# Kernel tuning notes

Hardware: AMD Instinct MI355X
Metric: run time of the kernel (lower is better)

Reference implementation:

```python
import jax, jax.numpy as jnp
import numpy as np

NOISE_STD = 0.5   # quantization_noise_std default in PSN.run
BETA = 0.25       # commitment-loss weight
B, E, C, K = 64, 256, 256, 8192


def setup_inputs() -> dict:
    key = jax.random.key(0)
    k1, k2, k3 = jax.random.split(key, 3)
    latents = jax.random.normal(k1, (B, E, C), dtype=jnp.float32)
    # initial_codebook: uniform(-1, 1) then mean-centered over the code axis
    codebook = jax.random.uniform(k2, (K, C), dtype=jnp.float32, minval=-1.0, maxval=1.0)
    codebook = codebook - codebook.mean(axis=0)
    noise = jax.random.normal(k3, (B * E, 1), dtype=jnp.float32)
    return {"latents": latents, "codebook": codebook, "noise": noise}


def reference(latents, codebook, noise):
    b, e, c = latents.shape
    k = codebook.shape[0]
    flat = latents.reshape(b * e, c)                      # (b s) (r c), r=1
    dist = (jnp.sum(flat * flat, axis=1, keepdims=True)
            + jnp.sum(codebook * codebook, axis=1)
            - 2.0 * jnp.matmul(flat, codebook.T))
    inds_det = jnp.argmin(dist, axis=1)                   # [N]
    offs = jnp.round(noise[:, 0] * NOISE_STD).astype(jnp.int32)
    inds_noisy = jnp.clip(inds_det.astype(jnp.int32) + offs, 0, k - 1)
    # one-hot @ codebook == gather (same math, same vjp scatter-add)
    q_det = codebook[inds_det].reshape(b, e, c)
    q_noisy = codebook[inds_noisy].reshape(b, e, c)
    # straight-through estimator output fed to the post-quantizer
    st = latents + jax.lax.stop_gradient(q_noisy - latents)
    # non_recon_loss(latents, q_det, q_noisy): beta*mse(latents, sg(q_det)) + mse(q_noisy, sg(latents))
    loss = (BETA * jnp.mean((latents - jax.lax.stop_gradient(q_det)) ** 2)
            + jnp.mean((q_noisy - jax.lax.stop_gradient(latents)) ** 2))
    return st, loss, inds_noisy.reshape(b, e)
```

## Files before the change

kernel.cpp:

```cpp
#include <hip/hip_runtime.h>
#include <hip/hip_bf16.h>


namespace {
constexpr int N_ROWS  = 16384;
constexpr int K_CODES = 8192;
constexpr int C_DIM   = 256;
constexpr float EPS_GAP = 0.004f;
}

typedef __attribute__((ext_vector_type(8)))  short bf16x8;
typedef __attribute__((ext_vector_type(16))) float f32x16;

typedef __attribute__((address_space(1))) const unsigned int gas_u32;
typedef __attribute__((address_space(3))) unsigned int las_u32;

__device__ __forceinline__ void gld16(const unsigned short* g, unsigned short* l) {
    __builtin_amdgcn_global_load_lds((gas_u32*)g, (las_u32*)l, 16, 0, 0);
}

__device__ __forceinline__ unsigned f2key(float f) {
    unsigned u = __float_as_uint(f);
    return (u & 0x80000000u) ? ~u : (u | 0x80000000u);
}
__device__ __forceinline__ float key2f(unsigned k) {
    unsigned u = (k & 0x80000000u) ? (k ^ 0x80000000u) : ~k;
    return __uint_as_float(u);
}
__device__ __forceinline__ unsigned short f2bf(float x) {
    unsigned u = __float_as_uint(x);
    unsigned r = u + 0x7fffu + ((u >> 16) & 1u);
    return (unsigned short)(r >> 16);
}

extern "C" __global__ void prep_kernel(const float* __restrict__ src,
                                       unsigned short* __restrict__ hi,
                                       unsigned short* __restrict__ lo) {
    const int i = (blockIdx.x * 256 + threadIdx.x) * 8;
    const int row = i >> 8, col = i & 255;
    const int d = (((row >> 5) * 8 + (col >> 5)) * 4 + ((col >> 3) & 3)) * 256
                + (row & 31) * 8;
    float4 a = *(const float4*)&src[i];
    float4 b = *(const float4*)&src[i + 4];
    float v[8] = {a.x, a.y, a.z, a.w, b.x, b.y, b.z, b.w};
    unsigned short h[8], l[8];
    #pragma unroll
    for (int j = 0; j < 8; ++j) {
        h[j] = f2bf(v[j]);
        float hf = __uint_as_float((unsigned)h[j] << 16);
        l[j] = f2bf(v[j] - hf);
    }
    ushort4 h0 = {h[0], h[1], h[2], h[3]}, h1 = {h[4], h[5], h[6], h[7]};
    ushort4 l0 = {l[0], l[1], l[2], l[3]}, l1 = {l[4], l[5], l[6], l[7]};
    *(ushort4*)&hi[d] = h0;  *(ushort4*)&hi[d + 4] = h1;
    *(ushort4*)&lo[d] = l0;  *(ushort4*)&lo[d + 4] = l1;
}

extern "C" __global__ void prepw_kernel(const float* __restrict__ src,
                                        unsigned short* __restrict__ hi,
                                        unsigned short* __restrict__ lo,
                                        float* __restrict__ wnorm) {
    const int i = (blockIdx.x * 256 + threadIdx.x) * 8;
    float4 a = *(const float4*)&src[i];
    float4 b = *(const float4*)&src[i + 4];
    float v[8] = {a.x, a.y, a.z, a.w, b.x, b.y, b.z, b.w};
    unsigned short h[8], l[8];
    float s = 0.0f;
    #pragma unroll
    for (int j = 0; j < 8; ++j) {
        h[j] = f2bf(v[j]);
        float hf = __uint_as_float((unsigned)h[j] << 16);
        l[j] = f2bf(v[j] - hf);
        s = fmaf(v[j], v[j], s);
    }
    ushort4 h0 = {h[0], h[1], h[2], h[3]}, h1 = {h[4], h[5], h[6], h[7]};
    ushort4 l0 = {l[0], l[1], l[2], l[3]}, l1 = {l[4], l[5], l[6], l[7]};
    *(ushort4*)&hi[i] = h0;  *(ushort4*)&hi[i + 4] = h1;
    *(ushort4*)&lo[i] = l0;  *(ushort4*)&lo[i + 4] = l1;
    #pragma unroll
    for (int m = 1; m < 32; m <<= 1) s += __shfl_xor(s, m, 64);
    if ((threadIdx.x & 31) == 0) wnorm[i >> 8] = s;
}

extern "C" __global__ void __launch_bounds__(256, 3)
pass1_kernel(const unsigned short* __restrict__ xh_g,
             const unsigned short* __restrict__ xl_g,
             const unsigned short* __restrict__ wh_g,
             const unsigned short* __restrict__ wl_g,
             const float* __restrict__ wnorm,
             unsigned long long* __restrict__ keys,
             unsigned* __restrict__ keys2) {
    __shared__ __align__(16) unsigned short LDS[2][2][128 * 32];
    const int tid = threadIdx.x;
    const int lane = tid & 63;
    const int wid = tid >> 6;
    const int h = lane >> 5;
    const int l31 = lane & 31;
    const int rb = blockIdx.x & 127, cs = blockIdx.x >> 7;
    const int r0 = rb * 128, cbase = cs * 512;

    const int dr = lane >> 2;
    const int gq = (lane & 3) ^ ((lane >> 3) & 3);
    const int laneoff = dr * 256 + gq * 8;

    const int fB = (l31 >> 1) & 3;

    const size_t abase = ((size_t)(rb * 4 + wid) * 8) * 1024 + h * 256 + l31 * 8;

    float bv[16];  unsigned bi[16];  float sv[16];
    #pragma unroll
    for (int r = 0; r < 16; ++r) { bv[r] = 3.4e38f; sv[r] = 3.4e38f; bi[r] = 0; }

    f32x16 acc[4];
    #pragma unroll
    for (int g = 0; g < 4; ++g)
        #pragma unroll
        for (int e = 0; e < 16; ++e) acc[g][e] = 0.0f;

    auto stageW = [&](int t, int b) {
        const int kc32 = (t & 7) * 32;
        const int cb = cbase + (t >> 3) * 128;
        #pragma unroll
        for (int c = 0; c < 2; ++c) {
            const int R = wid * 32 + c * 16;
            const size_t wg = (size_t)(cb + R) * 256 + kc32 + laneoff;
            gld16(wh_g + wg, &LDS[b][0][R * 32]);
            gld16(wl_g + wg, &LDS[b][1][R * 32]);
        }
    };

    bf16x8 cAh0, cAh1, cAl0, cAl1;
    bf16x8 nAh0, nAh1, nAl0, nAl1;

#define LOADA(H0, H1, L0, L1, tt)                                              \
    {   const size_t o_ = abase + (size_t)((tt) & 7) * 1024;                   \
        H0 = *(const bf16x8*)(xh_g + o_);                                      \
        H1 = *(const bf16x8*)(xh_g + o_ + 512);                                \
        L0 = *(const bf16x8*)(xl_g + o_);                                      \
        L1 = *(const bf16x8*)(xl_g + o_ + 512);                                \
    }

#define MFMA_TILE(H0, H1, L0, L1, P)                                           \
    {   _Pragma("unroll")                                                      \
        for (int kk = 0; kk < 2; ++kk) {                                       \
            const int q = kk * 2 + h;                                          \
            bf16x8 ah = kk ? H1 : H0;                                          \
            bf16x8 al = kk ? L1 : L0;                                          \
            _Pragma("unroll")                                                  \
            for (int g = 0; g < 4; ++g) {                                      \
                const int aB = (g * 32 + l31) * 32 + ((q ^ fB) << 3);          \
                bf16x8 bh = *(const bf16x8*)&LDS[P][0][aB];                    \
                bf16x8 bl = *(const bf16x8*)&LDS[P][1][aB];                    \
                acc[g] = __builtin_amdgcn_mfma_f32_32x32x16_bf16(ah, bh, acc[g], 0, 0, 0); \
                acc[g] = __builtin_amdgcn_mfma_f32_32x32x16_bf16(ah, bl, acc[g], 0, 0, 0); \
                acc[g] = __builtin_amdgcn_mfma_f32_32x32x16_bf16(al, bh, acc[g], 0, 0, 0); \
            }                                                                  \
        }                                                                      \
    }

    auto epilogue = [&](int t) {
        const int cb = cbase + (t >> 3) * 128;
        float wn0 = wnorm[cb + l31];
        float wn1 = wnorm[cb + 32 + l31];
        float wn2 = wnorm[cb + 64 + l31];
        float wn3 = wnorm[cb + 96 + l31];
        #pragma unroll
        for (int r = 0; r < 16; ++r) {
            #pragma unroll
            for (int g = 0; g < 4; ++g) {
                const float wn = g == 0 ? wn0 : g == 1 ? wn1 : g == 2 ? wn2 : wn3;
                float s = fmaf(-2.0f, acc[g][r], wn);
                bool c = s < bv[r];
                sv[r] = fminf(sv[r], c ? bv[r] : s);
                bv[r] = c ? s : bv[r];
                bi[r] = c ? (unsigned)(cb + g * 32 + l31) : bi[r];
            }
        }
        #pragma unroll
        for (int g = 0; g < 4; ++g)
            #pragma unroll
            for (int e = 0; e < 16; ++e) acc[g][e] = 0.0f;
    };

    stageW(0, 0);
    LOADA(cAh0, cAh1, cAl0, cAl1, 0);
    __syncthreads();
    for (int t2 = 0; t2 < 32; t2 += 2) {
        stageW(t2 + 1, 1);
        LOADA(nAh0, nAh1, nAl0, nAl1, t2 + 1);
        MFMA_TILE(cAh0, cAh1, cAl0, cAl1, 0);
        __syncthreads();

        if (t2 + 2 < 32) {
            stageW(t2 + 2, 0);
            LOADA(cAh0, cAh1, cAl0, cAl1, t2 + 2);
        }
        MFMA_TILE(nAh0, nAh1, nAl0, nAl1, 1);
        if (((t2 + 1) & 7) == 7) epilogue(t2 + 1);
        __syncthreads();
    }
#undef LOADA
#undef MFMA_TILE

    #pragma unroll
    for (int r = 0; r < 16; ++r) {
        unsigned long long key =
            ((unsigned long long)f2key(bv[r]) << 32) | bi[r];
        unsigned sk = f2key(sv[r]);
        #pragma unroll
        for (int m = 1; m < 32; m <<= 1) {
            unsigned long long ko = __shfl_xor(key, m, 64);
            unsigned sko = __shfl_xor(sk, m, 64);
            unsigned long long loser = key < ko ? ko : key;
            sk = min(min(sk, sko), (unsigned)(loser >> 32));
            key = key < ko ? key : ko;
        }
        if (l31 == 0) {
            const int grow = r0 + wid * 32 + (r & 3) + 8 * (r >> 2) + 4 * h;
            unsigned long long old = atomicMin(&keys[grow], key);
            if (old != ~0ull) {
                unsigned long long loser = old < key ? key : old;
                atomicMin(&keys2[grow], (unsigned)(loser >> 32));
            }
            atomicMin(&keys2[grow], sk);
        }
    }
}

extern "C" __global__ void flag_kernel(unsigned long long* __restrict__ keys,
                                       const unsigned* __restrict__ keys2,
                                       int* __restrict__ list, int* __restrict__ count) {
    const int row = blockIdx.x * 256 + threadIdx.x;
    unsigned long long k = keys[row];
    float b = key2f((unsigned)(k >> 32));
    float s = key2f(keys2[row]);
    if (s - b < EPS_GAP) {
        int p = atomicAdd(count, 1);
        list[p] = row;
        keys[row] = ~0ull;
    }
}

extern "C" __global__ void __launch_bounds__(256)
rerank_kernel(const float* __restrict__ lat,
              const float* __restrict__ cbk,
              const float* __restrict__ wnorm,
              const int* __restrict__ list,
              const int* __restrict__ count,
              unsigned long long* __restrict__ keys) {
    const int w = threadIdx.x >> 6, lane = threadIdx.x & 63;
    const int c0 = blockIdx.x * 16 + w * 4;
    float4 wv0 = *(const float4*)&cbk[(size_t)(c0 + 0) * C_DIM + lane * 4];
    float4 wv1 = *(const float4*)&cbk[(size_t)(c0 + 1) * C_DIM + lane * 4];
    float4 wv2 = *(const float4*)&cbk[(size_t)(c0 + 2) * C_DIM + lane * 4];
    float4 wv3 = *(const float4*)&cbk[(size_t)(c0 + 3) * C_DIM + lane * 4];
    const float wn0 = wnorm[c0 + 0], wn1 = wnorm[c0 + 1];
    const float wn2 = wnorm[c0 + 2], wn3 = wnorm[c0 + 3];
    const int n = *count;

    auto dot4 = [&](const float4& x, const float4& v) {
        float d = x.x * v.x;
        d = fmaf(x.y, v.y, d);
        d = fmaf(x.z, v.z, d);
        return fmaf(x.w, v.w, d);
    };
    auto best4 = [&](float a0, float a1, float a2, float a3) {
        unsigned long long k0 = ((unsigned long long)f2key(fmaf(-2.0f, a0, wn0)) << 32) | (unsigned)(c0 + 0);
        unsigned long long k1 = ((unsigned long long)f2key(fmaf(-2.0f, a1, wn1)) << 32) | (unsigned)(c0 + 1);
        unsigned long long k2 = ((unsigned long long)f2key(fmaf(-2.0f, a2, wn2)) << 32) | (unsigned)(c0 + 2);
        unsigned long long k3 = ((unsigned long long)f2key(fmaf(-2.0f, a3, wn3)) << 32) | (unsigned)(c0 + 3);
        unsigned long long b01 = k0 < k1 ? k0 : k1;
        unsigned long long b23 = k2 < k3 ? k2 : k3;
        return b01 < b23 ? b01 : b23;
    };

    int i = 0;
    for (; i + 2 <= n; i += 2) {
        const int r0 = list[i], r1 = list[i + 1];
        float4 x0 = *(const float4*)&lat[(size_t)r0 * C_DIM + lane * 4];
        float4 x1 = *(const float4*)&lat[(size_t)r1 * C_DIM + lane * 4];
        float d00 = dot4(x0, wv0), d01 = dot4(x0, wv1), d02 = dot4(x0, wv2), d03 = dot4(x0, wv3);
        float d10 = dot4(x1, wv0), d11 = dot4(x1, wv1), d12 = dot4(x1, wv2), d13 = dot4(x1, wv3);
        #pragma unroll
        for (int m = 1; m < 64; m <<= 1) {
            d00 += __shfl_xor(d00, m, 64); d01 += __shfl_xor(d01, m, 64);
            d02 += __shfl_xor(d02, m, 64); d03 += __shfl_xor(d03, m, 64);
            d10 += __shfl_xor(d10, m, 64); d11 += __shfl_xor(d11, m, 64);
            d12 += __shfl_xor(d12, m, 64); d13 += __shfl_xor(d13, m, 64);
        }
        if (lane == 0) {
            unsigned long long b0 = best4(d00, d01, d02, d03);
            unsigned long long b1 = best4(d10, d11, d12, d13);
            if (b0 < keys[r0]) atomicMin(&keys[r0], b0);
            if (b1 < keys[r1]) atomicMin(&keys[r1], b1);
        }
    }
    if (i < n) {
        const int r0 = list[i];
        float4 x0 = *(const float4*)&lat[(size_t)r0 * C_DIM + lane * 4];
        float d00 = dot4(x0, wv0), d01 = dot4(x0, wv1), d02 = dot4(x0, wv2), d03 = dot4(x0, wv3);
        #pragma unroll
        for (int m = 1; m < 64; m <<= 1) {
            d00 += __shfl_xor(d00, m, 64); d01 += __shfl_xor(d01, m, 64);
            d02 += __shfl_xor(d02, m, 64); d03 += __shfl_xor(d03, m, 64);
        }
        if (lane == 0) {
            unsigned long long b0 = best4(d00, d01, d02, d03);
            if (b0 < keys[r0]) atomicMin(&keys[r0], b0);
        }
    }
}

extern "C" __global__ void finalize_kernel(const float* __restrict__ lat,
                                           const float* __restrict__ cbk,
                                           const float* __restrict__ noise,
                                           const unsigned long long* __restrict__ keys,
                                           float* __restrict__ out,
                                           float* __restrict__ lpart) {
    const int g = threadIdx.x >> 5;
    const int l = threadIdx.x & 31;
    const int row = blockIdx.x * 8 + g;
    const unsigned long long p = keys[row];
    const int id = (int)(unsigned)(p & 0xFFFFFFFFull);
    const int off = (int)rintf(noise[row] * 0.5f);
    int idn = id + off;
    idn = idn < 0 ? 0 : (idn > K_CODES - 1 ? K_CODES - 1 : idn);
    const float4* latp = (const float4*)&lat[(size_t)row * C_DIM];
    const float4* qdp  = (const float4*)&cbk[(size_t)id  * C_DIM];
    const float4* qnp  = (const float4*)&cbk[(size_t)idn * C_DIM];
    float4* stp = (float4*)&out[(size_t)row * C_DIM];
    float t = 0.0f;
    #pragma unroll
    for (int j = 0; j < 2; ++j) {
        const int e = l + j * 32;
        float4 x  = latp[e];
        float4 qd = qdp[e];
        float4 qn = qnp[e];
        float4 st = {x.x + (qn.x - x.x), x.y + (qn.y - x.y),
                     x.z + (qn.z - x.z), x.w + (qn.w - x.w)};
        stp[e] = st;
        float d1, d2;
        d1 = x.x - qd.x; d2 = qn.x - x.x; t += 0.25f * d1 * d1 + d2 * d2;
        d1 = x.y - qd.y; d2 = qn.y - x.y; t += 0.25f * d1 * d1 + d2 * d2;
        d1 = x.z - qd.z; d2 = qn.z - x.z; t += 0.25f * d1 * d1 + d2 * d2;
        d1 = x.w - qd.w; d2 = qn.w - x.w; t += 0.25f * d1 * d1 + d2 * d2;
    }
    t *= (1.0f / 4194304.0f);
    #pragma unroll
    for (int m = 1; m < 32; m <<= 1) t += __shfl_xor(t, m, 64);
    __shared__ float red[8];
    if (l == 0) {
        red[g] = t;
        out[(size_t)N_ROWS * C_DIM + 1 + row] = (float)idn;
    }
    __syncthreads();
    if (threadIdx.x == 0) {
        float s = red[0] + red[1] + red[2] + red[3] + red[4] + red[5] + red[6] + red[7];
        atomicAdd(&lpart[blockIdx.x & 1023], s);
    }
}

extern "C" __global__ void loss_reduce_kernel(const float* __restrict__ lpart,
                                              float* __restrict__ out) {
    const int t = threadIdx.x;
    float s = lpart[t] + lpart[t + 256] + lpart[t + 512] + lpart[t + 768];
    #pragma unroll
    for (int m = 32; m; m >>= 1) s += __shfl_xor(s, m, 64);
    __shared__ float red[4];
    if ((t & 63) == 0) red[t >> 6] = s;
    __syncthreads();
    if (t == 0) out[(size_t)N_ROWS * C_DIM] = red[0] + red[1] + red[2] + red[3];
}

extern "C" void kernel_launch(void* const* d_in, const int* in_sizes, int n_in,
                              void* d_out, int out_size, void* d_ws, size_t ws_size,
                              hipStream_t stream) {
    const float* lat   = (const float*)d_in[0];
    const float* cbk   = (const float*)d_in[1];
    const float* noise = (const float*)d_in[2];
    float* out = (float*)d_out;

    char* ws = (char*)d_ws;
    unsigned short* xh = (unsigned short*)(ws);
    unsigned short* xl = (unsigned short*)(ws + 8388608);
    unsigned short* wh = (unsigned short*)(ws + 16777216);
    unsigned short* wl = (unsigned short*)(ws + 20971520);
    float* wnorm       = (float*)(ws + 25165824);
    unsigned long long* keys = (unsigned long long*)(ws + 25198592);
    unsigned* keys2    = (unsigned*)(ws + 25329664);
    int* list          = (int*)(ws + 25395200);
    float* lpart       = (float*)(ws + 25460736);
    int* count         = (int*)(ws + 25464832);

    hipMemsetAsync(keys, 0xFF, 192 * 1024, stream);
    hipMemsetAsync(lpart, 0, 4096 + 4, stream);

    prep_kernel <<<2048, 256, 0, stream>>>(lat, xh, xl);
    prepw_kernel<<<1024, 256, 0, stream>>>(cbk, wh, wl, wnorm);
    pass1_kernel<<<2048, 256, 0, stream>>>(xh, xl, wh, wl, wnorm, keys, keys2);
    flag_kernel <<<N_ROWS / 256, 256, 0, stream>>>(keys, keys2, list, count);
    rerank_kernel<<<K_CODES / 16, 256, 0, stream>>>(lat, cbk, wnorm, list, count, keys);
    finalize_kernel<<<N_ROWS / 8, 256, 0, stream>>>(lat, cbk, noise, keys, out, lpart);
    loss_reduce_kernel<<<1, 256, 0, stream>>>(lpart, out);
}
```

Before: 276.4 us.

## Triple-buffer codebook tiles in LDS with explicit waitcnt and scheduling barriers

Moves the codebook staging in the distance-GEMM pass from double to triple buffering, so weight tiles are prefetched two steps ahead. The full `__syncthreads` is replaced by a partial `s_waitcnt vmcnt(8)` plus a raw barrier, with `sched_barrier` fences to pin the load/MFMA order. The `wnorm` loads are hoisted out of the epilogue to the start of each 128-code group. The aim is to hide global-to-LDS latency behind MFMA work. In exchange, LDS per block grows by half, and the last iterations issue prefetches past the block's code range, which may read out of bounds for the final code slice.

Measured after the change: 283.1 us. 1.02x slower.

```diff
diff --git a/kernel.cpp b/kernel.cpp
--- a/kernel.cpp
+++ b/kernel.cpp
@@ -90,7 +90,7 @@
              const float* __restrict__ wnorm,
              unsigned long long* __restrict__ keys,
              unsigned* __restrict__ keys2) {
-    __shared__ __align__(16) unsigned short LDS[2][2][128 * 32];
+    __shared__ __align__(16) unsigned short LDS[3][2][128 * 32];
     const int tid = threadIdx.x;
     const int lane = tid & 63;
     const int wid = tid >> 6;
@@ -117,7 +117,8 @@
         #pragma unroll
         for (int e = 0; e < 16; ++e) acc[g][e] = 0.0f;
 
-    auto stageW = [&](int t, int b) {
+    auto stageW = [&](int t) {
+        const int b = t % 3;
         const int kc32 = (t & 7) * 32;
         const int cb = cbase + (t >> 3) * 128;
         #pragma unroll
@@ -131,6 +132,15 @@
 
     bf16x8 cAh0, cAh1, cAl0, cAl1;
     bf16x8 nAh0, nAh1, nAl0, nAl1;
+    float wn0 = 0, wn1 = 0, wn2 = 0, wn3 = 0;
+
+#define SCHED() __builtin_amdgcn_sched_barrier(0)
+#define WAITBAR()                                                              \
+    {   asm volatile("s_waitcnt vmcnt(8)" ::: "memory");                       \
+        SCHED();                                                               \
+        __builtin_amdgcn_s_barrier();                                          \
+        SCHED();                                                               \
+    }
 
 #define LOADA(H0, H1, L0, L1, tt)                                              \
     {   const size_t o_ = abase + (size_t)((tt) & 7) * 1024;                   \
@@ -160,10 +170,6 @@
 
     auto epilogue = [&](int t) {
         const int cb = cbase + (t >> 3) * 128;
-        float wn0 = wnorm[cb + l31];
-        float wn1 = wnorm[cb + 32 + l31];
-        float wn2 = wnorm[cb + 64 + l31];
-        float wn3 = wnorm[cb + 96 + l31];
         #pragma unroll
         for (int r = 0; r < 16; ++r) {
             #pragma unroll
@@ -182,25 +188,41 @@
             for (int e = 0; e < 16; ++e) acc[g][e] = 0.0f;
     };
 
-    stageW(0, 0);
+    stageW(0);
+    SCHED();
     LOADA(cAh0, cAh1, cAl0, cAl1, 0);
-    __syncthreads();
+    SCHED();
+    stageW(1);
+    WAITBAR();
+
     for (int t2 = 0; t2 < 32; t2 += 2) {
-        stageW(t2 + 1, 1);
+        if ((t2 & 7) == 0) {
+            const int cb = cbase + (t2 >> 3) * 128;
+            wn0 = wnorm[cb + l31];
+            wn1 = wnorm[cb + 32 + l31];
+            wn2 = wnorm[cb + 64 + l31];
+            wn3 = wnorm[cb + 96 + l31];
+        }
+        SCHED();
         LOADA(nAh0, nAh1, nAl0, nAl1, t2 + 1);
-        MFMA_TILE(cAh0, cAh1, cAl0, cAl1, 0);
-        __syncthreads();
-
-        if (t2 + 2 < 32) {
-            stageW(t2 + 2, 0);
-            LOADA(cAh0, cAh1, cAl0, cAl1, t2 + 2);
-        }
-        MFMA_TILE(nAh0, nAh1, nAl0, nAl1, 1);
+        SCHED();
+        stageW(t2 + 2);
+        SCHED();
+        MFMA_TILE(cAh0, cAh1, cAl0, cAl1, t2 % 3);
+        WAITBAR();
+
+        LOADA(cAh0, cAh1, cAl0, cAl1, t2 + 2);
+        SCHED();
+        stageW(t2 + 3);
+        SCHED();
+        MFMA_TILE(nAh0, nAh1, nAl0, nAl1, (t2 + 1) % 3);
         if (((t2 + 1) & 7) == 7) epilogue(t2 + 1);
-        __syncthreads();
+        WAITBAR();
     }
 #undef LOADA
 #undef MFMA_TILE
+#undef WAITBAR
+#undef SCHED
 
     #pragma unroll
     for (int r = 0; r < 16; ++r) {
```
